# Kernel tuning notes

Measured on AMD Instinct MI355X. Metric: run time of the kernel, lower is better.

Reference implementation:

```python
import jax, jax.numpy as jnp
import numpy as np

D_MODEL = 1024
N_HEADS = 16
HEAD_DIM = D_MODEL // N_HEADS  # 64


def _rotate_half(x):
    x1, x2 = jnp.split(x, 2, axis=-1)
    return jnp.concatenate((-x2, x1), axis=-1)


def setup_inputs() -> dict:
    key = jax.random.key(0)
    ks = jax.random.split(key, 9)
    B, S = 2, 2048
    sc = 1.0 / np.sqrt(D_MODEL)
    return {
        "x": jax.random.normal(ks[0], (B, S, D_MODEL), dtype=jnp.float32),
        "Wq": jax.random.normal(ks[1], (D_MODEL, D_MODEL), dtype=jnp.float32) * sc,
        "bq": jax.random.normal(ks[2], (D_MODEL,), dtype=jnp.float32) * 0.02,
        "Wk": jax.random.normal(ks[3], (D_MODEL, D_MODEL), dtype=jnp.float32) * sc,
        "bk": jax.random.normal(ks[4], (D_MODEL,), dtype=jnp.float32) * 0.02,
        "Wv": jax.random.normal(ks[5], (D_MODEL, D_MODEL), dtype=jnp.float32) * sc,
        "bv": jax.random.normal(ks[6], (D_MODEL,), dtype=jnp.float32) * 0.02,
        "Wo": jax.random.normal(ks[7], (D_MODEL, D_MODEL), dtype=jnp.float32) * sc,
        "bo": jax.random.normal(ks[8], (D_MODEL,), dtype=jnp.float32) * 0.02,
    }


def reference(x, Wq, bq, Wk, bk, Wv, bv, Wo, bo):
    B, S, _ = x.shape
    H, D = N_HEADS, HEAD_DIM
    # QKV projections -> [B, H, S, D]
    q = (x @ Wq + bq).reshape(B, S, H, D).transpose(0, 2, 1, 3)
    k = (x @ Wk + bk).reshape(B, S, H, D).transpose(0, 2, 1, 3)
    v = (x @ Wv + bv).reshape(B, S, H, D).transpose(0, 2, 1, 3)
    # Rotary embedding on head_dim
    inv_freq = 1.0 / (10000.0 ** (jnp.arange(0, D, 2, dtype=jnp.float32) / D))
    t = jnp.arange(S, dtype=jnp.float32)
    freqs = jnp.outer(t, inv_freq)                      # [S, D/2]
    emb = jnp.concatenate((freqs, freqs), axis=-1)      # [S, D]
    # Faithful to torch: cos/sin end up rank-5 [1,1,1,S,D], promoting q/k to [1,B,H,S,D]
    cos = jnp.cos(emb)[None, None, None]
    sin = jnp.sin(emb)[None, None, None]
    qe = q * cos + _rotate_half(q) * sin                # [1,B,H,S,D]
    ke = k * cos + _rotate_half(k) * sin                # [1,B,H,S,D]
    scores = jnp.matmul(qe, jnp.swapaxes(ke, -1, -2)) / np.sqrt(D).astype(np.float32)  # [1,B,H,S,S]
    attn = jax.nn.softmax(scores, axis=-1)
    out = jnp.matmul(attn, v)                           # [1,B,H,S,D] (v broadcast)
    # Faithful replication of torch transpose(1,2).contiguous().view(B,S,d_model)
    out = out.transpose(0, 2, 1, 3, 4).reshape(B, S, H * D)
    return out @ Wo + bo
```

## Files before the change

### kernel.cpp

```cpp
#include <hip/hip_runtime.h>
#include <hip/hip_bf16.h>
#include <stdint.h>

typedef __bf16 bf16;
typedef __bf16 bf16x8 __attribute__((ext_vector_type(8)));
typedef __bf16 bf16x4 __attribute__((ext_vector_type(4)));
typedef float  f32x4  __attribute__((ext_vector_type(4)));
typedef int    i32x4  __attribute__((ext_vector_type(4)));

#define MFMA16(a, b, c) __builtin_amdgcn_mfma_f32_16x16x32_bf16((a), (b), (c), 0, 0, 0)

#define GLOAD16(gp, lp) __builtin_amdgcn_global_load_lds(                     \
    (__attribute__((address_space(1))) void*)(gp),                            \
    (__attribute__((address_space(3))) void*)(lp), 16, 0, 0)


__global__ __launch_bounds__(256) void k_prep(
    const float* __restrict__ x,
    const float* __restrict__ Wq, const float* __restrict__ Wk,
    const float* __restrict__ Wv, const float* __restrict__ Wo,
    bf16* __restrict__ xb, bf16* __restrict__ wqkvt, bf16* __restrict__ wot,
    float* __restrict__ ct, float* __restrict__ st) {
    __shared__ float t[32][33];
    const int bid = blockIdx.x, tid = threadIdx.x;
    if (bid < 4096) {
        const int i = bid * 256 + tid;
        float4 v = ((const float4*)x)[i];
        bf16x4 o;
        o[0] = (bf16)v.x; o[1] = (bf16)v.y; o[2] = (bf16)v.z; o[3] = (bf16)v.w;
        ((bf16x4*)xb)[i] = o;
    } else if (bid < 4352) {
        const int i = (bid - 4096) * 256 + tid;
        const int s = i >> 5, j = i & 31;
        const float inv = expf(-(float)j * (9.210340371976184f / 32.0f));
        const float a = (float)s * inv;
        ct[i] = cosf(a);
        st[i] = sinf(a);
    } else {
        const int wb = bid - 4352;
        const int z = wb >> 10, tb = wb & 1023;
        const float* src = (z == 0) ? Wq : (z == 1) ? Wk : (z == 2) ? Wv : Wo;
        bf16* dst = (z < 3) ? wqkvt + (size_t)z * 1024 * 1024 : wot;
        const int bx = (tb & 31) * 32, by = (tb >> 5) * 32;
        const int tx = tid & 31, ty = tid >> 5;
#pragma unroll
        for (int i = 0; i < 32; i += 8)
            t[ty + i][tx] = src[(size_t)(by + ty + i) * 1024 + bx + tx];
        __syncthreads();
#pragma unroll
        for (int i = 0; i < 32; i += 8)
            dst[(size_t)(bx + ty + i) * 1024 + by + tx] = (bf16)t[tx][ty + i];
    }
}

__device__ __forceinline__ void gemm_loop(const bf16* __restrict__ A,
                                          const bf16* __restrict__ Bt,
                                          int m0, int n0,
                                          bf16* As, bf16* Bs,
                                          f32x4 (&acc)[4][4]) {
    const int tid  = threadIdx.x;
    const int w    = tid >> 6, lane = tid & 63;
    const int wr   = (w >> 1) * 64, wc = (w & 1) * 64;
    const int l15  = lane & 15, l4 = lane >> 4;
    const int srow = w * 16 + (lane >> 2);
    const int skol = 8 * ((lane & 3) ^ ((lane >> 3) & 3));
    const int rdb  = l15 * 32 + 8 * (l4 ^ ((l15 >> 1) & 3));
    const bf16* Ap = A  + (size_t)(m0 + srow) * 1024 + skol;
    const bf16* Bp = Bt + (size_t)(n0 + srow) * 1024 + skol;

#define GSTAGE(B, kt) do {                                                   \
        GLOAD16(Ap + (kt),         As + (B) * 4096 + w * 512);               \
        GLOAD16(Ap + 65536 + (kt), As + (B) * 4096 + 2048 + w * 512);        \
        GLOAD16(Bp + (kt),         Bs + (B) * 4096 + w * 512);               \
        GLOAD16(Bp + 65536 + (kt), Bs + (B) * 4096 + 2048 + w * 512);        \
    } while (0)

#define GTILE(t, B) do {                                                     \
        asm volatile("s_waitcnt vmcnt(0)" ::: "memory");                     \
        __builtin_amdgcn_s_barrier();                                        \
        if ((t) < 31) GSTAGE((B) ^ 1, ((t) + 1) * 32);                       \
        bf16x8 af[4], bfv[4];                                                \
        _Pragma("unroll")                                                    \
        for (int m = 0; m < 4; ++m)                                          \
            af[m] = *(const bf16x8*)(As + (B) * 4096 + (wr + 16 * m) * 32 + rdb); \
        _Pragma("unroll")                                                    \
        for (int n = 0; n < 4; ++n)                                          \
            bfv[n] = *(const bf16x8*)(Bs + (B) * 4096 + (wc + 16 * n) * 32 + rdb); \
        __builtin_amdgcn_s_setprio(1);                                       \
        _Pragma("unroll")                                                    \
        for (int m = 0; m < 4; ++m)                                          \
            _Pragma("unroll")                                                \
            for (int n = 0; n < 4; ++n)                                      \
                acc[m][n] = MFMA16(af[m], bfv[n], acc[m][n]);                \
        __builtin_amdgcn_s_setprio(0);                                       \
    } while (0)

    GSTAGE(0, 0);
    for (int t = 0; t < 32; t += 2) {
        GTILE(t, 0);
        GTILE(t + 1, 1);
    }
#undef GTILE
#undef GSTAGE
}

__global__ __launch_bounds__(256) void k_gemm_qkv(
    const bf16* __restrict__ X, const bf16* __restrict__ Wt,
    const float* __restrict__ bq, const float* __restrict__ bk,
    const float* __restrict__ bv,
    const float* __restrict__ ct, const float* __restrict__ st,
    bf16* __restrict__ qbuf, bf16* __restrict__ kbuf, bf16* __restrict__ vtb) {
    __shared__ __align__(16) bf16 As[2 * 4096];
    __shared__ __align__(16) bf16 Bs[2 * 4096];
    f32x4 acc[4][4] = {};
    const int nwg = gridDim.x * gridDim.y;
    const int wg  = blockIdx.y * gridDim.x + blockIdx.x;
    const int sw  = (wg & 7) * (nwg >> 3) + (wg >> 3);
    const int m0 = (sw / gridDim.x) * 128, n0 = (sw % gridDim.x) * 128;
    gemm_loop(X, Wt, m0, n0, As, Bs, acc);

    const int tid = threadIdx.x;
    const int w = tid >> 6, lane = tid & 63;
    const int wr = (w >> 1) * 64, wc = (w & 1) * 64;
    const int l15 = lane & 15, l4 = lane >> 4;

    const int featbase = n0 + wc;
    const int kind = featbase >> 10;
    const int col0 = featbase & 1023;
    const int h = col0 >> 6;
    const float* bias = (kind == 0) ? bq : (kind == 1) ? bk : bv;
    const float oscale = (kind == 0) ? 0.18033688011112042f : 1.0f;

#pragma unroll
    for (int m = 0; m < 4; ++m) {
#pragma unroll
        for (int j = 0; j < 4; ++j) {
            const int tok = m0 + wr + 16 * m + 4 * l4 + j;
            const int b = tok >> 11, s = tok & 2047;
            float vals[4];
#pragma unroll
            for (int n = 0; n < 4; ++n)
                vals[n] = acc[m][n][j] + bias[col0 + 16 * n + l15];
            if (kind < 2) {
                bf16* dst = (kind == 0) ? qbuf : kbuf;
                const size_t base = ((size_t)((b * 16 + h) * 2048 + s)) * 64;
#pragma unroll
                for (int n = 0; n < 4; ++n) {
                    const int dd = 16 * n + l15;
                    const int jr = dd & 31;
                    const float c = ct[s * 32 + jr], sn = st[s * 32 + jr];
                    const float other = vals[n ^ 2];
                    const float rot = (dd < 32) ? -other : other;
                    dst[base + dd] = (bf16)((vals[n] * c + rot * sn) * oscale);
                }
            } else {
                const int sp = (s & ~63) | ((s & 0x1C) << 1) | ((s & 0x20) >> 3) | (s & 3);
#pragma unroll
                for (int n = 0; n < 4; ++n) {
                    const int dd = 16 * n + l15;
                    vtb[((size_t)((b * 16 + h) * 64 + dd)) * 2048 + sp] = (bf16)vals[n];
                }
            }
        }
    }
}

__global__ __launch_bounds__(256) void k_attn(const bf16* __restrict__ qbuf,
                                              const bf16* __restrict__ kbuf,
                                              const bf16* __restrict__ vtb,
                                              bf16* __restrict__ ob) {
    __shared__ __align__(16) bf16 Ks[2 * 8192];
    __shared__ __align__(16) bf16 Vs[2 * 8192];

    const int tid = threadIdx.x, w = tid >> 6, lane = tid & 63;
    const int l15 = lane & 15, l4 = lane >> 4;

    const int sid = blockIdx.x;
    const int bh  = (sid & 7) * 4 + ((sid >> 3) >> 4);
    const int qb0 = ((sid >> 3) & 15) * 128;
    const int b = bh >> 4, h = bh & 15;

    const bf16* qp = qbuf + ((size_t)bh * 2048 + qb0 + w * 32 + l15) * 64 + 8 * l4;
    i32x4 qr00 = *(const i32x4*)qp;
    i32x4 qr01 = *(const i32x4*)(qp + 32);
    i32x4 qr10 = *(const i32x4*)(qp + 16 * 64);
    i32x4 qr11 = *(const i32x4*)(qp + 16 * 64 + 32);
    asm volatile("" :: "v"(qr00), "v"(qr01), "v"(qr10), "v"(qr11));
    asm volatile("s_waitcnt vmcnt(0)" ::: "memory");
    bf16x8 aq[2][2];
    aq[0][0] = __builtin_bit_cast(bf16x8, qr00);
    aq[0][1] = __builtin_bit_cast(bf16x8, qr01);
    aq[1][0] = __builtin_bit_cast(bf16x8, qr10);
    aq[1][1] = __builtin_bit_cast(bf16x8, qr11);

    bf16x8 ones;
#pragma unroll
    for (int i = 0; i < 8; ++i) ones[i] = (bf16)1.0f;

    f32x4 ao[2][4] = {};
    f32x4 lacc[2] = {};
    const f32x4 zf = {0.f, 0.f, 0.f, 0.f};

    const int r8   = lane >> 3;
    const int skol = 8 * ((lane & 7) ^ r8);
    const int rdb  = l15 * 64 + 32 * ((l15 >> 2) & 1) + 8 * (l4 ^ (l15 & 3));
    const bf16* kp = kbuf + (size_t)bh * 2048 * 64 + (size_t)(w * 8 + r8) * 64 + skol;
    const bf16* vp = vtb  + (size_t)bh * 64 * 2048 + (size_t)(w * 8 + r8) * 2048 + skol;

#define STAGE8(B, T) do {                                                         \
        GLOAD16(kp + (size_t)(2 * (T)) * 4096,            &Ks[(B) * 8192 + w * 512]);        \
        GLOAD16(kp + (size_t)(2 * (T)) * 4096 + 2048,     &Ks[(B) * 8192 + 2048 + w * 512]); \
        GLOAD16(kp + (size_t)(2 * (T) + 1) * 4096,        &Ks[(B) * 8192 + 4096 + w * 512]); \
        GLOAD16(kp + (size_t)(2 * (T) + 1) * 4096 + 2048, &Ks[(B) * 8192 + 6144 + w * 512]); \
        GLOAD16(vp + (2 * (T)) * 64,                      &Vs[(B) * 8192 + w * 512]);        \
        GLOAD16(vp + 65536 + (2 * (T)) * 64,              &Vs[(B) * 8192 + 2048 + w * 512]); \
        GLOAD16(vp + (2 * (T) + 1) * 64,                  &Vs[(B) * 8192 + 4096 + w * 512]); \
        GLOAD16(vp + 65536 + (2 * (T) + 1) * 64,          &Vs[(B) * 8192 + 6144 + w * 512]); \
    } while (0)

#define SUBT(B, SUB) do {                                                     \
        const bf16* Kb = &Ks[(B) * 8192 + (SUB) * 4096];                      \
        const bf16* Vb = &Vs[(B) * 8192 + (SUB) * 4096];                      \
        bf16x8 kfr[2][4], vfr[2][4];                                          \
        _Pragma("unroll")                                                     \
        for (int kk = 0; kk < 2; ++kk)                                        \
            _Pragma("unroll")                                                 \
            for (int n = 0; n < 4; ++n)                                       \
                kfr[kk][n] = *(const bf16x8*)(Kb + (rdb ^ (kk * 32)) + n * 1024); \
        _Pragma("unroll")                                                     \
        for (int kk = 0; kk < 2; ++kk)                                        \
            _Pragma("unroll")                                                 \
            for (int n = 0; n < 4; ++n)                                       \
                vfr[kk][n] = *(const bf16x8*)(Vb + (rdb ^ (kk * 32)) + n * 1024); \
        f32x4 sc[2][4];                                                       \
        __builtin_amdgcn_s_setprio(1);                                        \
        _Pragma("unroll")                                                     \
        for (int n = 0; n < 4; ++n) {                                         \
            sc[0][n] = MFMA16(kfr[0][n], aq[0][0], zf);                       \
            sc[1][n] = MFMA16(kfr[0][n], aq[1][0], zf);                       \
        }                                                                     \
        _Pragma("unroll")                                                     \
        for (int n = 0; n < 4; ++n) {                                         \
            sc[0][n] = MFMA16(kfr[1][n], aq[0][1], sc[0][n]);                 \
            sc[1][n] = MFMA16(kfr[1][n], aq[1][1], sc[1][n]);                 \
        }                                                                     \
        __builtin_amdgcn_s_setprio(0);                                        \
        bf16x8 ap[2][2];                                                      \
        _Pragma("unroll")                                                     \
        for (int f = 0; f < 2; ++f)                                           \
            _Pragma("unroll")                                                 \
            for (int r = 0; r < 4; ++r) {                                     \
                ap[f][0][r]     = (bf16)exp2f(sc[f][0][r]);                   \
                ap[f][1][r]     = (bf16)exp2f(sc[f][1][r]);                   \
                ap[f][0][4 + r] = (bf16)exp2f(sc[f][2][r]);                   \
                ap[f][1][4 + r] = (bf16)exp2f(sc[f][3][r]);                   \
            }                                                                 \
        __builtin_amdgcn_s_setprio(1);                                        \
        lacc[0] = MFMA16(ap[0][0], ones, lacc[0]);                            \
        lacc[0] = MFMA16(ap[0][1], ones, lacc[0]);                            \
        lacc[1] = MFMA16(ap[1][0], ones, lacc[1]);                            \
        lacc[1] = MFMA16(ap[1][1], ones, lacc[1]);                            \
        _Pragma("unroll")                                                     \
        for (int kk = 0; kk < 2; ++kk)                                        \
            _Pragma("unroll")                                                 \
            for (int n = 0; n < 4; ++n) {                                     \
                ao[0][n] = MFMA16(ap[0][kk], vfr[kk][n], ao[0][n]);           \
                ao[1][n] = MFMA16(ap[1][kk], vfr[kk][n], ao[1][n]);           \
            }                                                                 \
        __builtin_amdgcn_s_setprio(0);                                        \
    } while (0)

#define ATTILE(T, B) do {                                                     \
        asm volatile("s_waitcnt vmcnt(0)" ::: "memory");                      \
        __builtin_amdgcn_s_barrier();                                         \
        if ((T) < 15) STAGE8((B) ^ 1, (T) + 1);                               \
        SUBT(B, 0);                                                           \
        SUBT(B, 1);                                                           \
    } while (0)

    STAGE8(0, 0);
    for (int T = 0; T < 16; T += 2) {
        ATTILE(T, 0);
        ATTILE(T + 1, 1);
    }
#undef ATTILE
#undef SUBT
#undef STAGE8

#pragma unroll
    for (int f = 0; f < 2; ++f) {
#pragma unroll
        for (int j = 0; j < 4; ++j) {
            const float inv = 1.0f / lacc[f][j];
            const int s = qb0 + w * 32 + f * 16 + 4 * l4 + j;
            const size_t base = ((size_t)(h * 256 + b * 128 + (s >> 4))) * 1024 + (s & 15) * 64;
#pragma unroll
            for (int n = 0; n < 4; ++n)
                ob[base + 16 * n + l15] = (bf16)(ao[f][n][j] * inv);
        }
    }
}

__global__ __launch_bounds__(256) void k_gemm_out(const bf16* __restrict__ O,
                                                  const bf16* __restrict__ Wt,
                                                  const float* __restrict__ bo,
                                                  float* __restrict__ out) {
    __shared__ __align__(16) bf16 As[2 * 4096];
    __shared__ __align__(16) bf16 Bs[2 * 4096];
    f32x4 acc[4][4] = {};
    const int nwg = gridDim.x * gridDim.y;
    const int wg  = blockIdx.y * gridDim.x + blockIdx.x;
    const int sw  = (wg & 7) * (nwg >> 3) + (wg >> 3);
    const int m0 = (sw / gridDim.x) * 128, n0 = (sw % gridDim.x) * 128;
    gemm_loop(O, Wt, m0, n0, As, Bs, acc);

    const int tid = threadIdx.x;
    const int w = tid >> 6, lane = tid & 63;
    const int wr = (w >> 1) * 64, wc = (w & 1) * 64;
    const int l15 = lane & 15, l4 = lane >> 4;
#pragma unroll
    for (int m = 0; m < 4; ++m) {
#pragma unroll
        for (int j = 0; j < 4; ++j) {
            const int tok = m0 + wr + 16 * m + 4 * l4 + j;
#pragma unroll
            for (int n = 0; n < 4; ++n) {
                const int feat = n0 + wc + 16 * n + l15;
                out[(size_t)tok * 1024 + feat] = acc[m][n][j] + bo[feat];
            }
        }
    }
}

extern "C" void kernel_launch(void* const* d_in, const int* in_sizes, int n_in,
                              void* d_out, int out_size, void* d_ws, size_t ws_size,
                              hipStream_t stream) {
    (void)in_sizes; (void)n_in; (void)out_size; (void)ws_size;
    const float* x  = (const float*)d_in[0];
    const float* Wq = (const float*)d_in[1];
    const float* bq = (const float*)d_in[2];
    const float* Wk = (const float*)d_in[3];
    const float* bk = (const float*)d_in[4];
    const float* Wv = (const float*)d_in[5];
    const float* bv = (const float*)d_in[6];
    const float* Wo = (const float*)d_in[7];
    const float* bo = (const float*)d_in[8];
    float* out = (float*)d_out;

    char* p = (char*)d_ws;
    bf16* xb    = (bf16*)p;  p += (size_t)4096 * 1024 * 2;
    bf16* wqkvt = (bf16*)p;  p += (size_t)3072 * 1024 * 2;
    bf16* wot   = (bf16*)p;  p += (size_t)1024 * 1024 * 2;
    bf16* qbuf  = (bf16*)p;  p += (size_t)32 * 2048 * 64 * 2;
    bf16* kbuf  = (bf16*)p;  p += (size_t)32 * 2048 * 64 * 2;
    bf16* vtb   = (bf16*)p;  p += (size_t)32 * 64 * 2048 * 2;
    float* ct   = (float*)p; p += (size_t)2048 * 32 * 4;
    float* st   = (float*)p; p += (size_t)2048 * 32 * 4;
    bf16* obuf  = xb;

    k_prep<<<dim3(8448), dim3(256), 0, stream>>>(x, Wq, Wk, Wv, Wo,
                                                 xb, wqkvt, wot, ct, st);
    k_gemm_qkv<<<dim3(24, 32), dim3(256), 0, stream>>>(xb, wqkvt, bq, bk, bv,
                                                       ct, st, qbuf, kbuf, vtb);
    k_attn<<<dim3(512), dim3(256), 0, stream>>>(qbuf, kbuf, vtb, obuf);
    k_gemm_out<<<dim3(8, 32), dim3(256), 0, stream>>>(obuf, wot, bo, out);
}
```

Before: 136.0 us.

## Split attention KV range across two wave teams and merge partial results

The attention block grows from 256 to 512 threads. Two teams of four waves each handle half of the key/value sequence for the same 128 query rows, and their partial output and row-sum accumulators are merged through shared memory at the end. This doubles the waves in flight per block and halves each wave's serial loop length, which should hide latency better. The cost is an extra shared-memory reduction with barriers at the end, plus higher register pressure under launch_bounds(512,4). The merge needs no max rescale because the softmax is computed without a max subtraction.

Result: slower. 231.2 us (+69.9%).

```diff
diff --git a/kernel.cpp b/kernel.cpp
--- a/kernel.cpp
+++ b/kernel.cpp
@@ -165,14 +165,14 @@
     }
 }
 
-__global__ __launch_bounds__(256) void k_attn(const bf16* __restrict__ qbuf,
-                                              const bf16* __restrict__ kbuf,
-                                              const bf16* __restrict__ vtb,
-                                              bf16* __restrict__ ob) {
-    __shared__ __align__(16) bf16 Ks[2 * 8192];
-    __shared__ __align__(16) bf16 Vs[2 * 8192];
+__global__ __launch_bounds__(512, 4) void k_attn(const bf16* __restrict__ qbuf,
+                                                 const bf16* __restrict__ kbuf,
+                                                 const bf16* __restrict__ vtb,
+                                                 bf16* __restrict__ ob) {
+    __shared__ __align__(16) bf16 smem[2 * 2 * 2 * 4096];
 
     const int tid = threadIdx.x, w = tid >> 6, lane = tid & 63;
+    const int team = w >> 2, wt = w & 3;
     const int l15 = lane & 15, l4 = lane >> 4;
 
     const int sid = blockIdx.x;
@@ -180,7 +180,7 @@
     const int qb0 = ((sid >> 3) & 15) * 128;
     const int b = bh >> 4, h = bh & 15;
 
-    const bf16* qp = qbuf + ((size_t)bh * 2048 + qb0 + w * 32 + l15) * 64 + 8 * l4;
+    const bf16* qp = qbuf + ((size_t)bh * 2048 + qb0 + wt * 32 + l15) * 64 + 8 * l4;
     i32x4 qr00 = *(const i32x4*)qp;
     i32x4 qr01 = *(const i32x4*)(qp + 32);
     i32x4 qr10 = *(const i32x4*)(qp + 16 * 64);
@@ -204,34 +204,36 @@
     const int r8   = lane >> 3;
     const int skol = 8 * ((lane & 7) ^ r8);
     const int rdb  = l15 * 64 + 32 * ((l15 >> 2) & 1) + 8 * (l4 ^ (l15 & 3));
-    const bf16* kp = kbuf + (size_t)bh * 2048 * 64 + (size_t)(w * 8 + r8) * 64 + skol;
-    const bf16* vp = vtb  + (size_t)bh * 64 * 2048 + (size_t)(w * 8 + r8) * 2048 + skol;
-
-#define STAGE8(B, T) do {                                                         \
-        GLOAD16(kp + (size_t)(2 * (T)) * 4096,            &Ks[(B) * 8192 + w * 512]);        \
-        GLOAD16(kp + (size_t)(2 * (T)) * 4096 + 2048,     &Ks[(B) * 8192 + 2048 + w * 512]); \
-        GLOAD16(kp + (size_t)(2 * (T) + 1) * 4096,        &Ks[(B) * 8192 + 4096 + w * 512]); \
-        GLOAD16(kp + (size_t)(2 * (T) + 1) * 4096 + 2048, &Ks[(B) * 8192 + 6144 + w * 512]); \
-        GLOAD16(vp + (2 * (T)) * 64,                      &Vs[(B) * 8192 + w * 512]);        \
-        GLOAD16(vp + 65536 + (2 * (T)) * 64,              &Vs[(B) * 8192 + 2048 + w * 512]); \
-        GLOAD16(vp + (2 * (T) + 1) * 64,                  &Vs[(B) * 8192 + 4096 + w * 512]); \
-        GLOAD16(vp + 65536 + (2 * (T) + 1) * 64,          &Vs[(B) * 8192 + 6144 + w * 512]); \
+    const bf16* kp = kbuf + (size_t)bh * 131072 + (size_t)team * 65536
+                   + (size_t)(wt * 8 + r8) * 64 + skol;
+    const bf16* vp = vtb  + (size_t)bh * 131072 + (size_t)(wt * 8 + r8) * 2048
+                   + team * 1024 + skol;
+    bf16* sK = smem + team * 16384;
+    bf16* sV = smem + team * 16384 + 8192;
+    const bf16* pK0 = sK + rdb;
+    const bf16* pK1 = sK + (rdb ^ 32);
+    const bf16* pV0 = sV + rdb;
+    const bf16* pV1 = sV + (rdb ^ 32);
+
+#define STAGE(B, t) do {                                                  \
+        GLOAD16(kp + (size_t)(t) * 4096,        sK + (B) * 4096 + wt * 512);        \
+        GLOAD16(kp + (size_t)(t) * 4096 + 2048, sK + (B) * 4096 + 2048 + wt * 512); \
+        GLOAD16(vp + (t) * 64,                  sV + (B) * 4096 + wt * 512);        \
+        GLOAD16(vp + 65536 + (t) * 64,          sV + (B) * 4096 + 2048 + wt * 512); \
     } while (0)
 
-#define SUBT(B, SUB) do {                                                     \
-        const bf16* Kb = &Ks[(B) * 8192 + (SUB) * 4096];                      \
-        const bf16* Vb = &Vs[(B) * 8192 + (SUB) * 4096];                      \
+#define TILE(t, B) do {                                                       \
+        asm volatile("s_waitcnt vmcnt(0)" ::: "memory");                      \
+        __builtin_amdgcn_s_barrier();                                         \
+        if ((t) < 15) STAGE((B) ^ 1, (t) + 1);                                \
         bf16x8 kfr[2][4], vfr[2][4];                                          \
         _Pragma("unroll")                                                     \
-        for (int kk = 0; kk < 2; ++kk)                                        \
-            _Pragma("unroll")                                                 \
-            for (int n = 0; n < 4; ++n)                                       \
-                kfr[kk][n] = *(const bf16x8*)(Kb + (rdb ^ (kk * 32)) + n * 1024); \
-        _Pragma("unroll")                                                     \
-        for (int kk = 0; kk < 2; ++kk)                                        \
-            _Pragma("unroll")                                                 \
-            for (int n = 0; n < 4; ++n)                                       \
-                vfr[kk][n] = *(const bf16x8*)(Vb + (rdb ^ (kk * 32)) + n * 1024); \
+        for (int n = 0; n < 4; ++n) {                                         \
+            kfr[0][n] = *(const bf16x8*)(pK0 + (B) * 4096 + n * 1024);        \
+            kfr[1][n] = *(const bf16x8*)(pK1 + (B) * 4096 + n * 1024);        \
+            vfr[0][n] = *(const bf16x8*)(pV0 + (B) * 4096 + n * 1024);        \
+            vfr[1][n] = *(const bf16x8*)(pV1 + (B) * 4096 + n * 1024);        \
+        }                                                                     \
         f32x4 sc[2][4];                                                       \
         __builtin_amdgcn_s_setprio(1);                                        \
         _Pragma("unroll")                                                     \
@@ -270,33 +272,46 @@
         __builtin_amdgcn_s_setprio(0);                                        \
     } while (0)
 
-#define ATTILE(T, B) do {                                                     \
-        asm volatile("s_waitcnt vmcnt(0)" ::: "memory");                      \
-        __builtin_amdgcn_s_barrier();                                         \
-        if ((T) < 15) STAGE8((B) ^ 1, (T) + 1);                               \
-        SUBT(B, 0);                                                           \
-        SUBT(B, 1);                                                           \
-    } while (0)
-
-    STAGE8(0, 0);
-    for (int T = 0; T < 16; T += 2) {
-        ATTILE(T, 0);
-        ATTILE(T + 1, 1);
-    }
-#undef ATTILE
-#undef SUBT
-#undef STAGE8
-
-#pragma unroll
-    for (int f = 0; f < 2; ++f) {
-#pragma unroll
-        for (int j = 0; j < 4; ++j) {
-            const float inv = 1.0f / lacc[f][j];
-            const int s = qb0 + w * 32 + f * 16 + 4 * l4 + j;
-            const size_t base = ((size_t)(h * 256 + b * 128 + (s >> 4))) * 1024 + (s & 15) * 64;
-#pragma unroll
-            for (int n = 0; n < 4; ++n)
-                ob[base + 16 * n + l15] = (bf16)(ao[f][n][j] * inv);
+    STAGE(0, 0);
+    for (int t = 0; t < 16; t += 2) {
+        TILE(t, 0);
+        TILE(t + 1, 1);
+    }
+#undef TILE
+#undef STAGE
+
+    float* mO = (float*)(smem + 16384);
+    float* mL = (float*)smem;
+    __builtin_amdgcn_s_barrier();
+    if (team == 1) {
+#pragma unroll
+        for (int f = 0; f < 2; ++f) {
+#pragma unroll
+            for (int j = 0; j < 4; ++j) {
+                const int row = wt * 32 + f * 16 + 4 * l4 + j;
+#pragma unroll
+                for (int n = 0; n < 4; ++n)
+                    mO[row * 64 + 16 * n + l15] = ao[f][n][j];
+                if (l15 == 0) mL[row] = lacc[f][j];
+            }
+        }
+    }
+    __builtin_amdgcn_s_barrier();
+    if (team == 0) {
+#pragma unroll
+        for (int f = 0; f < 2; ++f) {
+#pragma unroll
+            for (int j = 0; j < 4; ++j) {
+                const int row = wt * 32 + f * 16 + 4 * l4 + j;
+                const float inv = 1.0f / (lacc[f][j] + mL[row]);
+                const int s = qb0 + row;
+                const size_t base = ((size_t)(h * 256 + b * 128 + (s >> 4))) * 1024
+                                  + (s & 15) * 64;
+#pragma unroll
+                for (int n = 0; n < 4; ++n)
+                    ob[base + 16 * n + l15] =
+                        (bf16)((ao[f][n][j] + mO[row * 64 + 16 * n + l15]) * inv);
+            }
         }
     }
 }
@@ -362,6 +377,6 @@
                                                  xb, wqkvt, wot, ct, st);
     k_gemm_qkv<<<dim3(24, 32), dim3(256), 0, stream>>>(xb, wqkvt, bq, bk, bv,
                                                        ct, st, qbuf, kbuf, vtb);
-    k_attn<<<dim3(512), dim3(256), 0, stream>>>(qbuf, kbuf, vtb, obuf);
+    k_attn<<<dim3(512), dim3(512), 0, stream>>>(qbuf, kbuf, vtb, obuf);
     k_gemm_out<<<dim3(8, 32), dim3(256), 0, stream>>>(obuf, wot, bo, out);
 }
```
